# Optimization experiments

Measured on AMD Instinct MI355X. Metric: run time of the kernel, lower is better.

## Reference

```python
import jax, jax.numpy as jnp
import numpy as np

B, S, D, F, E, NS, K = 2, 1024, 1024, 4096, 8, 8, 2
FS = F // NS  # shared-expert hidden size = d_ff // num_shared_experts


def setup_inputs() -> dict:
    key = jax.random.key(0)
    ks = jax.random.split(key, 8)
    scale = 0.02
    return {
        "hidden_states": jax.random.normal(ks[0], (B, S, D), jnp.float32),
        "gate_W": jax.random.normal(ks[1], (E, D), jnp.float32) * scale,
        "w1_e": jax.random.normal(ks[2], (E, D, F), jnp.float32) * scale,
        "w3_e": jax.random.normal(ks[3], (E, D, F), jnp.float32) * scale,
        "w2_e": jax.random.normal(ks[4], (E, F, D), jnp.float32) * scale,
        "w1_s": jax.random.normal(ks[5], (NS, D, FS), jnp.float32) * scale,
        "w3_s": jax.random.normal(ks[6], (NS, D, FS), jnp.float32) * scale,
        "w2_s": jax.random.normal(ks[7], (NS, FS, D), jnp.float32) * scale,
    }


def reference(hidden_states, gate_W, w1_e, w3_e, w2_e, w1_s, w3_s, w2_s):
    b, s, d = hidden_states.shape
    e = gate_W.shape[0]
    flat = hidden_states.reshape(-1, d)            # [T, D]
    T = flat.shape[0]

    # --- gate: softmax over experts, top-k probs scattered (k=0 slot only survives) ---
    logits = (flat @ gate_W.T).astype(jnp.float32)  # [T, E]
    probs = jax.nn.softmax(logits, axis=-1)
    top_v, top_i = jax.lax.top_k(probs, K)          # [T, K]
    gates = jnp.zeros((T, e), probs.dtype).at[jnp.arange(T)[:, None], top_i].set(top_v)

    # --- routed experts: module runs every expert densely on all tokens ---
    g = jax.nn.silu(jnp.einsum('td,edf->etf', flat, w1_e))  # [E, T, F]
    u = jnp.einsum('td,edf->etf', flat, w3_e)
    out_e = jnp.einsum('etf,efd->etd', g * u, w2_e)         # [E, T, D]
    routed = jnp.einsum('te,etd->td', gates, out_e).reshape(b, s, d)

    # --- shared experts (mean over NS experts) ---
    gs = jax.nn.silu(jnp.einsum('bsd,ndf->nbsf', hidden_states, w1_s))
    us = jnp.einsum('bsd,ndf->nbsf', hidden_states, w3_s)
    shared = jnp.einsum('nbsf,nfd->bsd', gs * us, w2_s) / w1_s.shape[0]

    alpha = 0.5
    return alpha * shared + (1.0 - alpha) * routed
```

## Files before the change

### kernel.cpp

```cpp
#include <hip/hip_runtime.h>

#define T 2048
#define D 1024
#define F 4096
#define E 8
#define NS 8
#define FS 512
#define SHB 5120
#define NROWS 7168
#define MT_MAX 56

typedef float floatx4 __attribute__((ext_vector_type(4)));
typedef short short8 __attribute__((ext_vector_type(8)));
typedef unsigned short ushort8v __attribute__((ext_vector_type(8)));

__device__ __forceinline__ unsigned short f2bf(float f) {
  unsigned int u = __float_as_uint(f);
  u += 0x7FFF + ((u >> 16) & 1);
  return (unsigned short)(u >> 16);
}

__device__ __forceinline__ void glds16(const void* g, void* l) {
  __builtin_amdgcn_global_load_lds(
      (const __attribute__((address_space(1))) void*)g,
      (__attribute__((address_space(3))) void*)l, 16, 0, 0);
}

__global__ void gate_kernel(const float* __restrict__ x, const float* __restrict__ gW,
                            unsigned short* __restrict__ xb, int* __restrict__ cnt,
                            int* __restrict__ list_tok, float* __restrict__ list_gate) {
  int t = blockIdx.x, tid = threadIdx.x;
  const float4* xr = (const float4*)(x + (size_t)t * D);
  const float4* g4 = (const float4*)gW;
  float4 xv = xr[tid];
  ushort4 xo;
  xo.x = f2bf(xv.x); xo.y = f2bf(xv.y); xo.z = f2bf(xv.z); xo.w = f2bf(xv.w);
  *(ushort4*)(xb + (size_t)t * D + tid * 4) = xo;
  float acc[E];
#pragma unroll
  for (int e = 0; e < E; ++e) {
    float4 w = g4[e * 256 + tid];
    acc[e] = xv.x * w.x + xv.y * w.y + xv.z * w.z + xv.w * w.w;
  }
#pragma unroll
  for (int o = 32; o > 0; o >>= 1)
#pragma unroll
    for (int e = 0; e < E; ++e) acc[e] += __shfl_down(acc[e], o, 64);
  __shared__ float wred[4][E];
  int lane = tid & 63, wv = tid >> 6;
  if (lane == 0)
#pragma unroll
    for (int e = 0; e < E; ++e) wred[wv][e] = acc[e];
  __syncthreads();
  if (tid == 0) {
    float l[E];
#pragma unroll
    for (int e = 0; e < E; ++e) l[e] = wred[0][e] + wred[1][e] + wred[2][e] + wred[3][e];
    int i1 = 0; float m1 = l[0];
    for (int e = 1; e < E; ++e) if (l[e] > m1) { m1 = l[e]; i1 = e; }
    int i2 = -1; float m2 = -3.4e38f;
    for (int e = 0; e < E; ++e) if (e != i1 && l[e] > m2) { m2 = l[e]; i2 = e; }
    float s = 0.f, p[E];
#pragma unroll
    for (int e = 0; e < E; ++e) { p[e] = __expf(l[e] - m1); s += p[e]; }
    float inv = 1.f / s;
    int p1 = atomicAdd(&cnt[i1], 1);
    list_tok[i1 * T + p1] = t; list_gate[i1 * T + p1] = p[i1] * inv;
    int p2 = atomicAdd(&cnt[i2], 1);
    list_tok[i2 * T + p2] = t; list_gate[i2 * T + p2] = p[i2] * inv;
  }
}

__global__ void offsets_kernel(const int* __restrict__ cnt, int* __restrict__ off,
                               int* __restrict__ mt_expert) {
  if (threadIdx.x == 0 && blockIdx.x == 0) {
    int o = 0;
    for (int e = 0; e < E; ++e) { off[e] = o; o += (cnt[e] + 127) & ~127; }
    off[E] = o;
    for (int i = 0; i < MT_MAX; ++i) mt_expert[i] = -1;
    for (int e = 0; e < E; ++e) {
      int t0 = off[e] >> 7, nt = (cnt[e] + 127) >> 7;
      for (int i = 0; i < nt; ++i) mt_expert[t0 + i] = e;
    }
    for (int i = SHB >> 7; i < MT_MAX; ++i) mt_expert[i] = E;
  }
}

__global__ void scatter_kernel(const int* __restrict__ cnt, const int* __restrict__ off,
                               const int* __restrict__ list_tok, const float* __restrict__ list_gate,
                               int* __restrict__ tok_of_row, float* __restrict__ row_scale,
                               int* __restrict__ tok_rows, int* __restrict__ tk) {
  int idx = blockIdx.x * 256 + threadIdx.x;
  int e = idx >> 11, i = idx & (T - 1);
  if (e < E && i < cnt[e]) {
    int row = off[e] + i;
    int t = list_tok[e * T + i];
    tok_of_row[row] = t;
    row_scale[row] = 0.5f * list_gate[e * T + i];
    int k = atomicAdd(&tk[t], 1);
    tok_rows[2 * t + k] = row;
  }
}

__device__ __forceinline__ void tc64(const float* __restrict__ in,
                                     unsigned short* __restrict__ out, int R, int C) {
  int r0 = blockIdx.y * 64, c0 = blockIdx.x * 64;
  __shared__ float tile[64][65];
  int tid = threadIdx.x;
  {
    int cl4 = (tid & 15) * 4;
    int rl0 = tid >> 4;
#pragma unroll
    for (int k = 0; k < 4; ++k) {
      int rl = rl0 + k * 16;
      float4 v = *(const float4*)(in + (size_t)(r0 + rl) * C + c0 + cl4);
      tile[rl][cl4] = v.x; tile[rl][cl4 + 1] = v.y;
      tile[rl][cl4 + 2] = v.z; tile[rl][cl4 + 3] = v.w;
    }
  }
  __syncthreads();
  {
    int cl = tid >> 2;
    int rq = tid & 3;
    int c = c0 + cl;
    int Rt = R >> 5;
    size_t cbase = ((size_t)(c >> 7) * Rt) * 4096 + (size_t)(c & 127) * 32;
#pragma unroll
    for (int s = 0; s < 2; ++s) {
      int rr = s * 32 + rq * 8;
      int r = r0 + rr;
      ushort8v v;
#pragma unroll
      for (int j = 0; j < 8; ++j) v[j] = f2bf(tile[rr + j][cl]);
      size_t o = cbase + (size_t)(r >> 5) * 4096 + (r & 31);
      *(ushort8v*)(out + o) = v;
    }
  }
}

__global__ void transpose_cast(const float* __restrict__ in, unsigned short* __restrict__ out,
                               int R, int C) {
  tc64(in + (size_t)blockIdx.z * R * C, out + (size_t)blockIdx.z * R * C, R, C);
}

__global__ void transpose_cast_pair(const float* __restrict__ inA, const float* __restrict__ inB,
                                    unsigned short* __restrict__ outA,
                                    unsigned short* __restrict__ outB, int R, int C) {
  int z = blockIdx.z, h = gridDim.z >> 1;
  const float* in = (z < h) ? inA : inB;
  unsigned short* out = (z < h) ? outA : outB;
  int zz = (z < h) ? z : z - h;
  tc64(in + (size_t)zz * R * C, out + (size_t)zz * R * C, R, C);
}

__global__ __launch_bounds__(256, 2) void up_gemm(
    const unsigned short* __restrict__ xb, const unsigned short* __restrict__ W1T,
    const unsigned short* __restrict__ W3T, const unsigned short* __restrict__ W1sT,
    const unsigned short* __restrict__ W3sT, const int* __restrict__ mt_expert,
    const int* __restrict__ tok_of_row, unsigned short* __restrict__ Hb) {
  int mt = blockIdx.y, ntile = blockIdx.x;
  int e = mt_expert[mt];
  if (e < 0) return;
  const unsigned short *B1, *B3;
  if (e < E) {
    B1 = W1T + (size_t)e * F * D;
    B3 = W3T + (size_t)e * F * D;
  } else {
    B1 = W1sT; B3 = W3sT;
  }
  __shared__ unsigned short Au0[128 * 32], B1u0[128 * 32], B3u0[128 * 32];
  __shared__ unsigned short Au1[128 * 32], B1u1[128 * 32], B3u1[128 * 32];
  __shared__ unsigned short Au2[128 * 32], B1u2[128 * 32], B3u2[128 * 32];
  int tid = threadIdx.x;
  int lane = tid & 63, wv = tid >> 6, wm = wv >> 1, wn = wv & 1;
  int row16 = lane & 15, quad = lane >> 4;
  int qsw8 = (quad ^ ((lane >> 1) & 3)) * 8;
  int swzb = (tid >> 2) * 64 + (((tid & 3) ^ ((tid >> 3) & 3)) * 16);
  int lw = wv * 1024;

  int r1 = tid >> 2;
  int hrow1 = mt * 128 + r1, hrow2 = hrow1 + 64;
  int srow1 = (e < E) ? tok_of_row[hrow1] : (hrow1 - SHB);
  int srow2 = (e < E) ? tok_of_row[hrow2] : (hrow2 - SHB);
  int asl = ((tid & 3) ^ ((tid >> 3) & 3)) * 16;
  const char* asrc1 = (const char*)(xb + (size_t)srow1 * D) + asl;
  const char* asrc2 = (const char*)(xb + (size_t)srow2 * D) + asl;
  const char* b1t = (const char*)(B1 + (size_t)ntile * (D / 32) * 4096);
  const char* b3t = (const char*)(B3 + (size_t)ntile * (D / 32) * 4096);

  floatx4 accg[4][4], accu[4][4];
#pragma unroll
  for (int i = 0; i < 4; ++i)
#pragma unroll
    for (int j = 0; j < 4; ++j) {
      accg[i][j] = (floatx4){0.f, 0.f, 0.f, 0.f};
      accu[i][j] = (floatx4){0.f, 0.f, 0.f, 0.f};
    }

  auto stage = [&](int kt, unsigned short* Ad, unsigned short* B1d, unsigned short* B3d) {
    size_t ko = (size_t)kt * 64;
    size_t bo = (size_t)kt * 8192;
    glds16(asrc1 + ko, (char*)Ad + lw);
    glds16(asrc2 + ko, (char*)Ad + 4096 + lw);
    glds16(b1t + bo + swzb, (char*)B1d + lw);
    glds16(b1t + bo + 4096 + swzb, (char*)B1d + 4096 + lw);
    glds16(b3t + bo + swzb, (char*)B3d + lw);
    glds16(b3t + bo + 4096 + swzb, (char*)B3d + 4096 + lw);
  };
  auto compute = [&](const unsigned short* Ac, const unsigned short* B1c,
                     const unsigned short* B3c) {
    short8 af[4], b1f[4], b3f[4];
#pragma unroll
    for (int mi = 0; mi < 4; ++mi)
      af[mi] = *(const short8*)(Ac + (wm * 64 + mi * 16 + row16) * 32 + qsw8);
#pragma unroll
    for (int ni = 0; ni < 4; ++ni) {
      b1f[ni] = *(const short8*)(B1c + (wn * 64 + ni * 16 + row16) * 32 + qsw8);
      b3f[ni] = *(const short8*)(B3c + (wn * 64 + ni * 16 + row16) * 32 + qsw8);
    }
#pragma unroll
    for (int mi = 0; mi < 4; ++mi)
#pragma unroll
      for (int ni = 0; ni < 4; ++ni) {
        accg[mi][ni] = __builtin_amdgcn_mfma_f32_16x16x32_bf16(af[mi], b1f[ni], accg[mi][ni], 0, 0, 0);
        accu[mi][ni] = __builtin_amdgcn_mfma_f32_16x16x32_bf16(af[mi], b3f[ni], accu[mi][ni], 0, 0, 0);
      }
  };

  stage(0, Au0, B1u0, B3u0);
  stage(1, Au1, B1u1, B3u1);
  asm volatile("s_waitcnt vmcnt(6)" ::: "memory");
  __builtin_amdgcn_s_barrier();
  for (int t = 0; t < 30; t += 3) {
    stage(t + 2, Au2, B1u2, B3u2);
    compute(Au0, B1u0, B3u0);
    asm volatile("s_waitcnt vmcnt(6)" ::: "memory");
    __builtin_amdgcn_s_barrier();
    stage(t + 3, Au0, B1u0, B3u0);
    compute(Au1, B1u1, B3u1);
    asm volatile("s_waitcnt vmcnt(6)" ::: "memory");
    __builtin_amdgcn_s_barrier();
    stage(t + 4, Au1, B1u1, B3u1);
    compute(Au2, B1u2, B3u2);
    asm volatile("s_waitcnt vmcnt(6)" ::: "memory");
    __builtin_amdgcn_s_barrier();
  }
  compute(Au0, B1u0, B3u0);
  asm volatile("s_waitcnt vmcnt(0)" ::: "memory");
  __builtin_amdgcn_s_barrier();
  compute(Au1, B1u1, B3u1);

#pragma unroll
  for (int mi = 0; mi < 4; ++mi)
#pragma unroll
    for (int ni = 0; ni < 4; ++ni)
#pragma unroll
      for (int r = 0; r < 4; ++r) {
        int hrow = mt * 128 + wm * 64 + mi * 16 + quad * 4 + r;
        int col = ntile * 128 + wn * 64 + ni * 16 + row16;
        float g = accg[mi][ni][r], u = accu[mi][ni][r];
        float h = g * u / (1.0f + __expf(-g));
        size_t o = ((size_t)(hrow >> 7) * 128 + (col >> 5)) * 4096 + (size_t)(hrow & 127) * 32 + (col & 31);
        Hb[o] = f2bf(h);
      }
}

__global__ __launch_bounds__(256, 2) void down_gemm(
    const unsigned short* __restrict__ Hb, const unsigned short* __restrict__ W2T,
    const unsigned short* __restrict__ W2sT, const int* __restrict__ mt_expert,
    const float* __restrict__ row_scale, float* __restrict__ O) {
  int mt = blockIdx.y, ntile = blockIdx.x;
  int e = mt_expert[mt];
  if (e < 0) return;
  const char* Bt = (const char*)(((e < E) ? (W2T + (size_t)e * D * F) : W2sT)
                                 + (size_t)ntile * (F / 32) * 4096);
  const char* At = (const char*)(Hb + (size_t)mt * (F / 32) * 4096);
  __shared__ unsigned short Ad0[128 * 32], Bd0[128 * 32];
  __shared__ unsigned short Ad1[128 * 32], Bd1[128 * 32];
  __shared__ unsigned short Ad2[128 * 32], Bd2[128 * 32];
  int tid = threadIdx.x;
  int lane = tid & 63, wv = tid >> 6, wm = wv >> 1, wn = wv & 1;
  int row16 = lane & 15, quad = lane >> 4;
  int qsw8 = (quad ^ ((lane >> 1) & 3)) * 8;
  int swzb = (tid >> 2) * 64 + (((tid & 3) ^ ((tid >> 3) & 3)) * 16);
  int lw = wv * 1024;
  floatx4 acc[4][4];
#pragma unroll
  for (int i = 0; i < 4; ++i)
#pragma unroll
    for (int j = 0; j < 4; ++j) acc[i][j] = (floatx4){0.f, 0.f, 0.f, 0.f};

  auto stage = [&](int kt, unsigned short* Ad, unsigned short* Bd) {
    size_t o = (size_t)kt * 8192;
    glds16(At + o + swzb, (char*)Ad + lw);
    glds16(At + o + 4096 + swzb, (char*)Ad + 4096 + lw);
    glds16(Bt + o + swzb, (char*)Bd + lw);
    glds16(Bt + o + 4096 + swzb, (char*)Bd + 4096 + lw);
  };
  auto compute = [&](const unsigned short* Ac, const unsigned short* Bc) {
    short8 af[4], bf[4];
#pragma unroll
    for (int mi = 0; mi < 4; ++mi)
      af[mi] = *(const short8*)(Ac + (wm * 64 + mi * 16 + row16) * 32 + qsw8);
#pragma unroll
    for (int ni = 0; ni < 4; ++ni)
      bf[ni] = *(const short8*)(Bc + (wn * 64 + ni * 16 + row16) * 32 + qsw8);
#pragma unroll
    for (int mi = 0; mi < 4; ++mi)
#pragma unroll
      for (int ni = 0; ni < 4; ++ni)
        acc[mi][ni] = __builtin_amdgcn_mfma_f32_16x16x32_bf16(af[mi], bf[ni], acc[mi][ni], 0, 0, 0);
  };

  stage(0, Ad0, Bd0);
  stage(1, Ad1, Bd1);
  asm volatile("s_waitcnt vmcnt(4)" ::: "memory");
  __builtin_amdgcn_s_barrier();
  for (int t = 0; t < 126; t += 3) {
    stage(t + 2, Ad2, Bd2);
    compute(Ad0, Bd0);
    asm volatile("s_waitcnt vmcnt(4)" ::: "memory");
    __builtin_amdgcn_s_barrier();
    stage(t + 3, Ad0, Bd0);
    compute(Ad1, Bd1);
    asm volatile("s_waitcnt vmcnt(4)" ::: "memory");
    __builtin_amdgcn_s_barrier();
    stage(t + 4, Ad1, Bd1);
    compute(Ad2, Bd2);
    asm volatile("s_waitcnt vmcnt(4)" ::: "memory");
    __builtin_amdgcn_s_barrier();
  }
  compute(Ad0, Bd0);
  asm volatile("s_waitcnt vmcnt(0)" ::: "memory");
  __builtin_amdgcn_s_barrier();
  compute(Ad1, Bd1);

#pragma unroll
  for (int mi = 0; mi < 4; ++mi)
#pragma unroll
    for (int ni = 0; ni < 4; ++ni)
#pragma unroll
      for (int r = 0; r < 4; ++r) {
        int grow = mt * 128 + wm * 64 + mi * 16 + quad * 4 + r;
        int col = ntile * 128 + wn * 64 + ni * 16 + row16;
        float scale = (grow < SHB) ? row_scale[grow] : 0.0625f;
        O[(size_t)grow * D + col] = acc[mi][ni][r] * scale;
      }
}

__global__ void combine_kernel(const float* __restrict__ O, const int* __restrict__ tok_rows,
                               float* __restrict__ out) {
  int idx = blockIdx.x * 256 + threadIdx.x;
  int t = idx >> 8, c = idx & 255;
  int r0 = tok_rows[2 * t], r1 = tok_rows[2 * t + 1];
  const float4* O4 = (const float4*)O;
  float4 a = O4[(size_t)r0 * 256 + c];
  float4 b = O4[(size_t)r1 * 256 + c];
  float4 s = O4[((size_t)SHB + t) * 256 + c];
  float4 r;
  r.x = a.x + b.x + s.x;
  r.y = a.y + b.y + s.y;
  r.z = a.z + b.z + s.z;
  r.w = a.w + b.w + s.w;
  ((float4*)out)[idx] = r;
}

extern "C" void kernel_launch(void* const* d_in, const int* in_sizes, int n_in,
                              void* d_out, int out_size, void* d_ws, size_t ws_size,
                              hipStream_t stream) {
  (void)in_sizes; (void)n_in; (void)out_size; (void)ws_size;
  const float* x   = (const float*)d_in[0];
  const float* gW  = (const float*)d_in[1];
  const float* w1e = (const float*)d_in[2];
  const float* w3e = (const float*)d_in[3];
  const float* w2e = (const float*)d_in[4];
  const float* w1s = (const float*)d_in[5];
  const float* w3s = (const float*)d_in[6];
  const float* w2s = (const float*)d_in[7];
  float* out = (float*)d_out;

  char* w = (char*)d_ws;
  auto alloc = [&](size_t bytes) {
    char* p = w; w += (bytes + 255) & ~(size_t)255; return p;
  };
  unsigned short* xb   = (unsigned short*)alloc((size_t)T * D * 2);
  unsigned short* W1T  = (unsigned short*)alloc((size_t)E * F * D * 2);
  unsigned short* W3T  = (unsigned short*)alloc((size_t)E * F * D * 2);
  unsigned short* W2T  = (unsigned short*)alloc((size_t)E * D * F * 2);
  unsigned short* W1sT = (unsigned short*)alloc((size_t)F * D * 2);
  unsigned short* W3sT = (unsigned short*)alloc((size_t)F * D * 2);
  unsigned short* W2sT = (unsigned short*)alloc((size_t)D * F * 2);
  unsigned short* Hb   = (unsigned short*)alloc((size_t)NROWS * F * 2);
  float* Ob        = (float*)alloc((size_t)NROWS * D * 4);
  float* row_scale = (float*)alloc((size_t)SHB * 4);
  float* list_gate = (float*)alloc((size_t)E * T * 4);
  int* list_tok    = (int*)alloc((size_t)E * T * 4);
  int* tok_rows    = (int*)alloc((size_t)T * 2 * 4);
  int* offv        = (int*)alloc(16 * 4);
  int* mt_expert   = (int*)alloc(64 * 4);
  int* ctrl        = (int*)alloc((size_t)(8 + T + SHB) * 4);
  int* cnt = ctrl; int* tk = ctrl + 8; int* tok_of_row = ctrl + 8 + T;

  hipMemsetAsync(ctrl, 0, (size_t)(8 + T + SHB) * 4, stream);
  gate_kernel<<<T, 256, 0, stream>>>(x, gW, xb, cnt, list_tok, list_gate);
  offsets_kernel<<<1, 64, 0, stream>>>(cnt, offv, mt_expert);
  scatter_kernel<<<(E * T) / 256, 256, 0, stream>>>(cnt, offv, list_tok, list_gate,
                                                    tok_of_row, row_scale, tok_rows, tk);
  transpose_cast_pair<<<dim3(F / 64, D / 64, 2 * E), 256, 0, stream>>>(w1e, w3e, W1T, W3T, D, F);
  transpose_cast<<<dim3(D / 64, F / 64, E), 256, 0, stream>>>(w2e, W2T, F, D);
  transpose_cast_pair<<<dim3(FS / 64, D / 64, 2 * NS), 256, 0, stream>>>(w1s, w3s, W1sT, W3sT, D, FS);
  transpose_cast<<<dim3(D / 64, F / 64, 1), 256, 0, stream>>>(w2s, W2sT, F, D);
  up_gemm<<<dim3(F / 128, MT_MAX), 256, 0, stream>>>(xb, W1T, W3T, W1sT, W3sT,
                                                     mt_expert, tok_of_row, Hb);
  down_gemm<<<dim3(D / 128, MT_MAX), 256, 0, stream>>>(Hb, W2T, W2sT, mt_expert, row_scale, Ob);
  combine_kernel<<<(T * D / 4) / 256, 256, 0, stream>>>(Ob, tok_rows, out);
}
```

Baseline: 698.3 us.

## Fuse gate and weight transposes into one prep kernel; derive routing inline

Merges the gate kernel and the four weight transpose-cast launches into a single flat-grid prep kernel. It also removes the offsets and scatter kernels by having the GEMMs and combine recompute expert segment offsets from the per-expert counts. Tokens and gates are read straight from the per-expert lists, and each token records its expert and slot in an assign array. This cuts several launches, one larger memset and the scatter pass, at the cost of a little per-block prefix-sum work in the GEMMs and combine.

New measurement: 666.3 us. 1.05x faster.

```diff
diff --git a/kernel.cpp b/kernel.cpp
--- a/kernel.cpp
+++ b/kernel.cpp
@@ -26,10 +26,71 @@
       (__attribute__((address_space(3))) void*)l, 16, 0, 0);
 }
 
-__global__ void gate_kernel(const float* __restrict__ x, const float* __restrict__ gW,
-                            unsigned short* __restrict__ xb, int* __restrict__ cnt,
-                            int* __restrict__ list_tok, float* __restrict__ list_gate) {
-  int t = blockIdx.x, tid = threadIdx.x;
+__device__ __forceinline__ int route(const int* __restrict__ cnt, int r0b,
+                                     int& obase, int& ccnt) {
+  int e = -1, o = 0, ob = 0, cc = 0;
+#pragma unroll
+  for (int i = 0; i < E; ++i) {
+    int c = cnt[i];
+    int p = (c + 127) & ~127;
+    if (r0b >= o && r0b < o + p) { e = i; ob = o; cc = c; }
+    o += p;
+  }
+  if (r0b >= SHB) e = E;
+  obase = ob; ccnt = cc;
+  return e;
+}
+
+__device__ __forceinline__ int seg_off(const int* __restrict__ cnt, int e) {
+  int o = 0;
+#pragma unroll
+  for (int i = 0; i < E; ++i) { int p = (cnt[i] + 127) & ~127; o += (i < e) ? p : 0; }
+  return o;
+}
+
+__device__ __forceinline__ void tc64(const float* __restrict__ in,
+                                     unsigned short* __restrict__ out, int R, int C,
+                                     int bx, int by, float tile[64][65]) {
+  int r0 = by * 64, c0 = bx * 64;
+  int tid = threadIdx.x;
+  {
+    int cl4 = (tid & 15) * 4;
+    int rl0 = tid >> 4;
+#pragma unroll
+    for (int k = 0; k < 4; ++k) {
+      int rl = rl0 + k * 16;
+      float4 v = *(const float4*)(in + (size_t)(r0 + rl) * C + c0 + cl4);
+      tile[rl][cl4] = v.x; tile[rl][cl4 + 1] = v.y;
+      tile[rl][cl4 + 2] = v.z; tile[rl][cl4 + 3] = v.w;
+    }
+  }
+  __syncthreads();
+  {
+    int cl = tid >> 2, rq = tid & 3;
+    int c = c0 + cl;
+    int Rt = R >> 5;
+    size_t cbase = ((size_t)(c >> 7) * Rt) * 4096 + (size_t)(c & 127) * 32;
+#pragma unroll
+    for (int s = 0; s < 2; ++s) {
+      int rr = s * 32 + rq * 8;
+      int r = r0 + rr;
+      ushort8v v;
+#pragma unroll
+      for (int j = 0; j < 8; ++j) v[j] = f2bf(tile[rr + j][cl]);
+      size_t o = cbase + (size_t)(r >> 5) * 4096 + (r & 31);
+      *(ushort8v*)(out + o) = v;
+    }
+  }
+}
+
+__device__ __forceinline__ void gate_body(const float* __restrict__ x,
+                                          const float* __restrict__ gW,
+                                          unsigned short* __restrict__ xb,
+                                          int* __restrict__ cnt,
+                                          int* __restrict__ list_tok,
+                                          float* __restrict__ list_gate,
+                                          int* __restrict__ assign, int t, float* wred) {
+  int tid = threadIdx.x;
   const float4* xr = (const float4*)(x + (size_t)t * D);
   const float4* g4 = (const float4*)gW;
   float4 xv = xr[tid];
@@ -46,16 +107,15 @@
   for (int o = 32; o > 0; o >>= 1)
 #pragma unroll
     for (int e = 0; e < E; ++e) acc[e] += __shfl_down(acc[e], o, 64);
-  __shared__ float wred[4][E];
   int lane = tid & 63, wv = tid >> 6;
   if (lane == 0)
 #pragma unroll
-    for (int e = 0; e < E; ++e) wred[wv][e] = acc[e];
+    for (int e = 0; e < E; ++e) wred[wv * E + e] = acc[e];
   __syncthreads();
   if (tid == 0) {
     float l[E];
 #pragma unroll
-    for (int e = 0; e < E; ++e) l[e] = wred[0][e] + wred[1][e] + wred[2][e] + wred[3][e];
+    for (int e = 0; e < E; ++e) l[e] = wred[0 * E + e] + wred[1 * E + e] + wred[2 * E + e] + wred[3 * E + e];
     int i1 = 0; float m1 = l[0];
     for (int e = 1; e < E; ++e) if (l[e] > m1) { m1 = l[e]; i1 = e; }
     int i2 = -1; float m2 = -3.4e38f;
@@ -66,100 +126,59 @@
     float inv = 1.f / s;
     int p1 = atomicAdd(&cnt[i1], 1);
     list_tok[i1 * T + p1] = t; list_gate[i1 * T + p1] = p[i1] * inv;
+    assign[2 * t] = (i1 << 16) | p1;
     int p2 = atomicAdd(&cnt[i2], 1);
     list_tok[i2 * T + p2] = t; list_gate[i2 * T + p2] = p[i2] * inv;
-  }
-}
-
-__global__ void offsets_kernel(const int* __restrict__ cnt, int* __restrict__ off,
-                               int* __restrict__ mt_expert) {
-  if (threadIdx.x == 0 && blockIdx.x == 0) {
-    int o = 0;
-    for (int e = 0; e < E; ++e) { off[e] = o; o += (cnt[e] + 127) & ~127; }
-    off[E] = o;
-    for (int i = 0; i < MT_MAX; ++i) mt_expert[i] = -1;
-    for (int e = 0; e < E; ++e) {
-      int t0 = off[e] >> 7, nt = (cnt[e] + 127) >> 7;
-      for (int i = 0; i < nt; ++i) mt_expert[t0 + i] = e;
-    }
-    for (int i = SHB >> 7; i < MT_MAX; ++i) mt_expert[i] = E;
-  }
-}
-
-__global__ void scatter_kernel(const int* __restrict__ cnt, const int* __restrict__ off,
-                               const int* __restrict__ list_tok, const float* __restrict__ list_gate,
-                               int* __restrict__ tok_of_row, float* __restrict__ row_scale,
-                               int* __restrict__ tok_rows, int* __restrict__ tk) {
-  int idx = blockIdx.x * 256 + threadIdx.x;
-  int e = idx >> 11, i = idx & (T - 1);
-  if (e < E && i < cnt[e]) {
-    int row = off[e] + i;
-    int t = list_tok[e * T + i];
-    tok_of_row[row] = t;
-    row_scale[row] = 0.5f * list_gate[e * T + i];
-    int k = atomicAdd(&tk[t], 1);
-    tok_rows[2 * t + k] = row;
-  }
-}
-
-__device__ __forceinline__ void tc64(const float* __restrict__ in,
-                                     unsigned short* __restrict__ out, int R, int C) {
-  int r0 = blockIdx.y * 64, c0 = blockIdx.x * 64;
+    assign[2 * t + 1] = (i2 << 16) | p2;
+  }
+}
+
+__global__ void prep_kernel(const float* __restrict__ x, const float* __restrict__ gW,
+                            const float* __restrict__ w1e, const float* __restrict__ w3e,
+                            const float* __restrict__ w2e, const float* __restrict__ w1s,
+                            const float* __restrict__ w3s, const float* __restrict__ w2s,
+                            unsigned short* __restrict__ W1T, unsigned short* __restrict__ W3T,
+                            unsigned short* __restrict__ W2T, unsigned short* __restrict__ W1sT,
+                            unsigned short* __restrict__ W3sT, unsigned short* __restrict__ W2sT,
+                            unsigned short* __restrict__ xb, int* __restrict__ cnt,
+                            int* __restrict__ list_tok, float* __restrict__ list_gate,
+                            int* __restrict__ assign) {
   __shared__ float tile[64][65];
-  int tid = threadIdx.x;
-  {
-    int cl4 = (tid & 15) * 4;
-    int rl0 = tid >> 4;
-#pragma unroll
-    for (int k = 0; k < 4; ++k) {
-      int rl = rl0 + k * 16;
-      float4 v = *(const float4*)(in + (size_t)(r0 + rl) * C + c0 + cl4);
-      tile[rl][cl4] = v.x; tile[rl][cl4 + 1] = v.y;
-      tile[rl][cl4 + 2] = v.z; tile[rl][cl4 + 3] = v.w;
-    }
-  }
-  __syncthreads();
-  {
-    int cl = tid >> 2;
-    int rq = tid & 3;
-    int c = c0 + cl;
-    int Rt = R >> 5;
-    size_t cbase = ((size_t)(c >> 7) * Rt) * 4096 + (size_t)(c & 127) * 32;
-#pragma unroll
-    for (int s = 0; s < 2; ++s) {
-      int rr = s * 32 + rq * 8;
-      int r = r0 + rr;
-      ushort8v v;
-#pragma unroll
-      for (int j = 0; j < 8; ++j) v[j] = f2bf(tile[rr + j][cl]);
-      size_t o = cbase + (size_t)(r >> 5) * 4096 + (r & 31);
-      *(ushort8v*)(out + o) = v;
-    }
-  }
-}
-
-__global__ void transpose_cast(const float* __restrict__ in, unsigned short* __restrict__ out,
-                               int R, int C) {
-  tc64(in + (size_t)blockIdx.z * R * C, out + (size_t)blockIdx.z * R * C, R, C);
-}
-
-__global__ void transpose_cast_pair(const float* __restrict__ inA, const float* __restrict__ inB,
-                                    unsigned short* __restrict__ outA,
-                                    unsigned short* __restrict__ outB, int R, int C) {
-  int z = blockIdx.z, h = gridDim.z >> 1;
-  const float* in = (z < h) ? inA : inB;
-  unsigned short* out = (z < h) ? outA : outB;
-  int zz = (z < h) ? z : z - h;
-  tc64(in + (size_t)zz * R * C, out + (size_t)zz * R * C, R, C);
+  int bid = blockIdx.x;
+  if (bid < 24576) {
+    int seg = bid >> 13;
+    int t = bid & 8191;
+    int z = t >> 10, rem = t & 1023;
+    if (seg == 0)
+      tc64(w1e + (size_t)z * D * F, W1T + (size_t)z * D * F, D, F, rem & 63, rem >> 6, tile);
+    else if (seg == 1)
+      tc64(w3e + (size_t)z * D * F, W3T + (size_t)z * D * F, D, F, rem & 63, rem >> 6, tile);
+    else
+      tc64(w2e + (size_t)z * F * D, W2T + (size_t)z * F * D, F, D, rem & 15, rem >> 4, tile);
+  } else if (bid < 26624) {
+    int t = bid - 24576;
+    int seg = t >> 10, tt = t & 1023;
+    int z = tt >> 7, rem = tt & 127;
+    if (seg == 0)
+      tc64(w1s + (size_t)z * D * FS, W1sT + (size_t)z * D * FS, D, FS, rem & 7, rem >> 3, tile);
+    else
+      tc64(w3s + (size_t)z * D * FS, W3sT + (size_t)z * D * FS, D, FS, rem & 7, rem >> 3, tile);
+  } else if (bid < 27648) {
+    int rem = bid - 26624;
+    tc64(w2s, W2sT, F, D, rem & 15, rem >> 4, tile);
+  } else {
+    gate_body(x, gW, xb, cnt, list_tok, list_gate, assign, bid - 27648, (float*)tile);
+  }
 }
 
 __global__ __launch_bounds__(256, 2) void up_gemm(
     const unsigned short* __restrict__ xb, const unsigned short* __restrict__ W1T,
     const unsigned short* __restrict__ W3T, const unsigned short* __restrict__ W1sT,
-    const unsigned short* __restrict__ W3sT, const int* __restrict__ mt_expert,
-    const int* __restrict__ tok_of_row, unsigned short* __restrict__ Hb) {
+    const unsigned short* __restrict__ W3sT, const int* __restrict__ cnt,
+    const int* __restrict__ list_tok, unsigned short* __restrict__ Hb) {
   int mt = blockIdx.y, ntile = blockIdx.x;
-  int e = mt_expert[mt];
+  int obase, ccnt;
+  int e = route(cnt, mt * 128, obase, ccnt);
   if (e < 0) return;
   const unsigned short *B1, *B3;
   if (e < E) {
@@ -180,8 +199,15 @@
 
   int r1 = tid >> 2;
   int hrow1 = mt * 128 + r1, hrow2 = hrow1 + 64;
-  int srow1 = (e < E) ? tok_of_row[hrow1] : (hrow1 - SHB);
-  int srow2 = (e < E) ? tok_of_row[hrow2] : (hrow2 - SHB);
+  int srow1, srow2;
+  if (e < E) {
+    int i1 = hrow1 - obase; i1 = (i1 < ccnt) ? i1 : ccnt - 1;
+    int i2 = hrow2 - obase; i2 = (i2 < ccnt) ? i2 : ccnt - 1;
+    srow1 = list_tok[e * T + i1];
+    srow2 = list_tok[e * T + i2];
+  } else {
+    srow1 = hrow1 - SHB; srow2 = hrow2 - SHB;
+  }
   int asl = ((tid & 3) ^ ((tid >> 3) & 3)) * 16;
   const char* asrc1 = (const char*)(xb + (size_t)srow1 * D) + asl;
   const char* asrc2 = (const char*)(xb + (size_t)srow2 * D) + asl;
@@ -267,10 +293,11 @@
 
 __global__ __launch_bounds__(256, 2) void down_gemm(
     const unsigned short* __restrict__ Hb, const unsigned short* __restrict__ W2T,
-    const unsigned short* __restrict__ W2sT, const int* __restrict__ mt_expert,
-    const float* __restrict__ row_scale, float* __restrict__ O) {
+    const unsigned short* __restrict__ W2sT, const int* __restrict__ cnt,
+    const float* __restrict__ list_gate, float* __restrict__ O) {
   int mt = blockIdx.y, ntile = blockIdx.x;
-  int e = mt_expert[mt];
+  int obase, ccnt;
+  int e = route(cnt, mt * 128, obase, ccnt);
   if (e < 0) return;
   const char* Bt = (const char*)(((e < E) ? (W2T + (size_t)e * D * F) : W2sT)
                                  + (size_t)ntile * (F / 32) * 4096);
@@ -343,16 +370,24 @@
       for (int r = 0; r < 4; ++r) {
         int grow = mt * 128 + wm * 64 + mi * 16 + quad * 4 + r;
         int col = ntile * 128 + wn * 64 + ni * 16 + row16;
-        float scale = (grow < SHB) ? row_scale[grow] : 0.0625f;
+        float scale;
+        if (e < E) {
+          int i = grow - obase;
+          scale = (i < ccnt) ? 0.5f * list_gate[e * T + i] : 0.0f;
+        } else {
+          scale = 0.0625f;
+        }
         O[(size_t)grow * D + col] = acc[mi][ni][r] * scale;
       }
 }
 
-__global__ void combine_kernel(const float* __restrict__ O, const int* __restrict__ tok_rows,
-                               float* __restrict__ out) {
+__global__ void combine_kernel(const float* __restrict__ O, const int* __restrict__ cnt,
+                               const int* __restrict__ assign, float* __restrict__ out) {
   int idx = blockIdx.x * 256 + threadIdx.x;
   int t = idx >> 8, c = idx & 255;
-  int r0 = tok_rows[2 * t], r1 = tok_rows[2 * t + 1];
+  int a0 = assign[2 * t], a1 = assign[2 * t + 1];
+  int r0 = seg_off(cnt, a0 >> 16) + (a0 & 0xFFFF);
+  int r1 = seg_off(cnt, a1 >> 16) + (a1 & 0xFFFF);
   const float4* O4 = (const float4*)O;
   float4 a = O4[(size_t)r0 * 256 + c];
   float4 b = O4[(size_t)r1 * 256 + c];
@@ -392,26 +427,17 @@
   unsigned short* W2sT = (unsigned short*)alloc((size_t)D * F * 2);
   unsigned short* Hb   = (unsigned short*)alloc((size_t)NROWS * F * 2);
   float* Ob        = (float*)alloc((size_t)NROWS * D * 4);
-  float* row_scale = (float*)alloc((size_t)SHB * 4);
   float* list_gate = (float*)alloc((size_t)E * T * 4);
   int* list_tok    = (int*)alloc((size_t)E * T * 4);
-  int* tok_rows    = (int*)alloc((size_t)T * 2 * 4);
-  int* offv        = (int*)alloc(16 * 4);
-  int* mt_expert   = (int*)alloc(64 * 4);
-  int* ctrl        = (int*)alloc((size_t)(8 + T + SHB) * 4);
-  int* cnt = ctrl; int* tk = ctrl + 8; int* tok_of_row = ctrl + 8 + T;
-
-  hipMemsetAsync(ctrl, 0, (size_t)(8 + T + SHB) * 4, stream);
-  gate_kernel<<<T, 256, 0, stream>>>(x, gW, xb, cnt, list_tok, list_gate);
-  offsets_kernel<<<1, 64, 0, stream>>>(cnt, offv, mt_expert);
-  scatter_kernel<<<(E * T) / 256, 256, 0, stream>>>(cnt, offv, list_tok, list_gate,
-                                                    tok_of_row, row_scale, tok_rows, tk);
-  transpose_cast_pair<<<dim3(F / 64, D / 64, 2 * E), 256, 0, stream>>>(w1e, w3e, W1T, W3T, D, F);
-  transpose_cast<<<dim3(D / 64, F / 64, E), 256, 0, stream>>>(w2e, W2T, F, D);
-  transpose_cast_pair<<<dim3(FS / 64, D / 64, 2 * NS), 256, 0, stream>>>(w1s, w3s, W1sT, W3sT, D, FS);
-  transpose_cast<<<dim3(D / 64, F / 64, 1), 256, 0, stream>>>(w2s, W2sT, F, D);
+  int* assign      = (int*)alloc((size_t)T * 2 * 4);
+  int* cnt         = (int*)alloc(E * 4);
+
+  hipMemsetAsync(cnt, 0, E * 4, stream);
+  prep_kernel<<<29696, 256, 0, stream>>>(x, gW, w1e, w3e, w2e, w1s, w3s, w2s,
+                                         W1T, W3T, W2T, W1sT, W3sT, W2sT,
+                                         xb, cnt, list_tok, list_gate, assign);
   up_gemm<<<dim3(F / 128, MT_MAX), 256, 0, stream>>>(xb, W1T, W3T, W1sT, W3sT,
-                                                     mt_expert, tok_of_row, Hb);
-  down_gemm<<<dim3(D / 128, MT_MAX), 256, 0, stream>>>(Hb, W2T, W2sT, mt_expert, row_scale, Ob);
-  combine_kernel<<<(T * D / 4) / 256, 256, 0, stream>>>(Ob, tok_rows, out);
-}
+                                                     cnt, list_tok, Hb);
+  down_gemm<<<dim3(D / 128, MT_MAX), 256, 0, stream>>>(Hb, W2T, W2sT, cnt, list_gate, Ob);
+  combine_kernel<<<(T * D / 4) / 256, 256, 0, stream>>>(Ob, cnt, assign, out);
+}
```
